# Performance work log

Measured on AMD Instinct MI355X. Metric: run time of the kernel, lower is better.

Reference implementation:

```python
import jax, jax.numpy as jnp
import numpy as np

NEG_SLOPE = 0.2
EPS = 1e-12


def setup_inputs() -> dict:
    key = jax.random.key(0)
    k1, k2, k3, k4, k5 = jax.random.split(key, 5)
    N, E, IN, OUT = 100000, 1600000, 256, 64
    x = jax.random.normal(k1, (N, IN), dtype=jnp.float32)
    edge_index = jax.random.randint(k2, (2, E), 0, N, dtype=jnp.int64)
    # GATConv (heads=1) parameters: lin weight, att_src, att_dst, bias
    W = jax.random.normal(k3, (IN, OUT), dtype=jnp.float32) * (1.0 / np.sqrt(IN))
    att_src = jax.random.normal(k4, (OUT,), dtype=jnp.float32) * (1.0 / np.sqrt(OUT))
    att_dst = jax.random.normal(k5, (OUT,), dtype=jnp.float32) * (1.0 / np.sqrt(OUT))
    bias = jnp.zeros((OUT,), dtype=jnp.float32)
    return {"x": x, "edge_index": edge_index, "W": W,
            "att_src": att_src, "att_dst": att_dst, "bias": bias}


def reference(x, edge_index, W, att_src, att_dst, bias):
    N = x.shape[0]
    # PyG GATConv default add_self_loops=True
    loops = jnp.arange(N, dtype=edge_index.dtype)
    src = jnp.concatenate([edge_index[0], loops])  # source j of edge (j -> i)
    dst = jnp.concatenate([edge_index[1], loops])  # target i (softmax segment)

    h = x @ W                                      # [N, out]
    a_src = h @ att_src                            # [N] per-node source score
    a_dst = h @ att_dst                            # [N] per-node target score

    e = jax.nn.leaky_relu(a_src[src] + a_dst[dst], NEG_SLOPE)  # [E+N]
    # segment softmax over incoming edges of each destination node
    e_max = jax.ops.segment_max(e, dst, num_segments=N)
    e = jnp.exp(e - e_max[dst])
    denom = jax.ops.segment_sum(e, dst, num_segments=N)
    alpha = e / denom[dst]                         # [E+N]

    # scatter-aggregate: out[i] = sum_j alpha_ij * h[j]
    out = jax.ops.segment_sum(alpha[:, None] * h[src], dst, num_segments=N)
    out = out + bias

    # dropout (p=0.3) in eval mode is identity; then F.normalize (row-wise L2)
    nrm = jnp.sqrt(jnp.sum(out * out, axis=-1, keepdims=True))
    return out / jnp.maximum(nrm, EPS)
```

## Files before the change

kernel.cpp:

```cpp
#include <hip/hip_runtime.h>
#include <hip/hip_bf16.h>
#include <math.h>

#define NEG_SLOPE 0.2f
#define EPS_NRM 1e-12f
#define K_IN 256
#define C_OUT 64

typedef __attribute__((ext_vector_type(8))) short bf16x8;
typedef __attribute__((ext_vector_type(4))) float f32x4;

__device__ __forceinline__ unsigned short bf16_rne(float v) {
    unsigned u = __float_as_uint(v);
    return (unsigned short)((u + 0x7fffu + ((u >> 16) & 1u)) >> 16);
}

__global__ __launch_bounds__(256) void wsplit(
    const float* __restrict__ W, unsigned short* __restrict__ Wt_hi,
    unsigned short* __restrict__ Wt_lo)
{
    int tid = blockIdx.x * blockDim.x + threadIdx.x;
    if (tid >= K_IN * C_OUT) return;
    int k = tid >> 6, c = tid & 63;
    float v = W[tid];
    unsigned short hb = bf16_rne(v);
    float vh = __uint_as_float((unsigned)hb << 16);
    unsigned short lb = bf16_rne(v - vh);
    Wt_hi[c * K_IN + k] = hb;
    Wt_lo[c * K_IN + k] = lb;
}

__global__ __launch_bounds__(256) void gemm_att(
    const float* __restrict__ x,
    const unsigned short* __restrict__ Wt_hi,
    const unsigned short* __restrict__ Wt_lo,
    const float* __restrict__ att_s, const float* __restrict__ att_d,
    __hip_bfloat16* __restrict__ h, float* __restrict__ a_src_arr,
    float* __restrict__ a_dst_arr, int N,
    const int* __restrict__ dstA, int* __restrict__ cnt, int E)
{
    int t   = threadIdx.x;
    int gw  = (blockIdx.x * blockDim.x + t) >> 6;
    int l   = t & 63;
    int lm  = l & 15;
    int grp = l >> 4;
    int row0 = gw * 16;

    int srow = row0 + lm; if (srow >= N) srow = N - 1;
    const float* xq = x + (size_t)srow * K_IN + grp * 8;

    const unsigned short* wbh = Wt_hi + (size_t)lm * K_IN + grp * 8;
    const unsigned short* wbl = Wt_lo + (size_t)lm * K_IN + grp * 8;

    f32x4 acc[4];
#pragma unroll
    for (int n = 0; n < 4; ++n) acc[n] = (f32x4){0.f, 0.f, 0.f, 0.f};

    float4 xa = *(const float4*)(xq);
    float4 xb = *(const float4*)(xq + 4);

    for (int kt = 0; kt < K_IN / 32; ++kt) {
        float4 xa2, xb2;
        if (kt < K_IN / 32 - 1) {
            xa2 = *(const float4*)(xq + (kt + 1) * 32);
            xb2 = *(const float4*)(xq + (kt + 1) * 32 + 4);
        }
        short sh[8], sl[8];
        const float* fa = (const float*)&xa;
        const float* fb = (const float*)&xb;
#pragma unroll
        for (int i = 0; i < 4; ++i) {
            float v0 = fa[i], v1 = fb[i];
            unsigned short h0 = bf16_rne(v0), h1 = bf16_rne(v1);
            sh[i] = (short)h0; sh[i + 4] = (short)h1;
            sl[i]     = (short)bf16_rne(v0 - __uint_as_float((unsigned)h0 << 16));
            sl[i + 4] = (short)bf16_rne(v1 - __uint_as_float((unsigned)h1 << 16));
        }
        bf16x8 xh = *(bf16x8*)&sh[0];
        bf16x8 xl = *(bf16x8*)&sl[0];

        int ko = kt * 32;
#pragma unroll
        for (int n = 0; n < 4; ++n) {
            bf16x8 wh = *(const bf16x8*)(wbh + (size_t)n * 16 * K_IN + ko);
            bf16x8 wl = *(const bf16x8*)(wbl + (size_t)n * 16 * K_IN + ko);
            acc[n] = __builtin_amdgcn_mfma_f32_16x16x32_bf16(wh, xh, acc[n], 0, 0, 0);
            acc[n] = __builtin_amdgcn_mfma_f32_16x16x32_bf16(wl, xh, acc[n], 0, 0, 0);
            acc[n] = __builtin_amdgcn_mfma_f32_16x16x32_bf16(wh, xl, acc[n], 0, 0, 0);
        }
        xa = xa2; xb = xb2;
    }

    int row = row0 + lm;
    float ps = 0.f, pd = 0.f;
#pragma unroll
    for (int n = 0; n < 4; ++n) {
        float4 as4 = *(const float4*)(att_s + n * 16 + grp * 4);
        float4 ad4 = *(const float4*)(att_d + n * 16 + grp * 4);
        f32x4 a = acc[n];
        ps += a.x * as4.x + a.y * as4.y + a.z * as4.z + a.w * as4.w;
        pd += a.x * ad4.x + a.y * ad4.y + a.z * ad4.z + a.w * ad4.w;
    }
    ps += __shfl_xor(ps, 16, 64); ps += __shfl_xor(ps, 32, 64);
    pd += __shfl_xor(pd, 16, 64); pd += __shfl_xor(pd, 32, 64);
    if (row < N) {
        if (grp == 0) { a_src_arr[row] = ps; a_dst_arr[row] = pd; }
#pragma unroll
        for (int n = 0; n < 4; ++n) {
            f32x4 a = acc[n];
            __hip_bfloat16 b0 = __float2bfloat16(a.x);
            __hip_bfloat16 b1 = __float2bfloat16(a.y);
            __hip_bfloat16 b2 = __float2bfloat16(a.z);
            __hip_bfloat16 b3 = __float2bfloat16(a.w);
            unsigned long long pk =
                (unsigned long long)*(unsigned short*)&b0 |
                ((unsigned long long)*(unsigned short*)&b1 << 16) |
                ((unsigned long long)*(unsigned short*)&b2 << 32) |
                ((unsigned long long)*(unsigned short*)&b3 << 48);
            *(unsigned long long*)(h + (size_t)row * C_OUT + n * 16 + grp * 4) = pk;
        }
    }

    int stride = gridDim.x * blockDim.x;
    for (int i = blockIdx.x * blockDim.x + t; i < E; i += stride)
        atomicAdd(&cnt[dstA[i]], 1);
}

__global__ __launch_bounds__(256) void scan_p1(
    const int* __restrict__ cnt, int* __restrict__ partials, int n)
{
    int b = blockIdx.x, t = threadIdx.x;
    int base = b * 1024;
    int s = 0;
#pragma unroll
    for (int j = 0; j < 4; ++j) {
        int i = base + t * 4 + j;
        if (i < n) s += cnt[i];
    }
    for (int d = 1; d < 64; d <<= 1) s += __shfl_xor(s, d, 64);
    __shared__ int wsum[4];
    int lane = t & 63, wid = t >> 6;
    if (lane == 0) wsum[wid] = s;
    __syncthreads();
    if (t == 0) partials[b] = wsum[0] + wsum[1] + wsum[2] + wsum[3];
}

__global__ __launch_bounds__(256) void scan_p2(int* partials, int nb)
{
    __shared__ int buf[256];
    int t = threadIdx.x;
    int v = (t < nb) ? partials[t] : 0;
    buf[t] = v;
    __syncthreads();
    for (int d = 1; d < 256; d <<= 1) {
        int w = (t >= d) ? buf[t - d] : 0;
        __syncthreads();
        buf[t] += w;
        __syncthreads();
    }
    if (t < nb) partials[t] = buf[t] - v;
}

__global__ __launch_bounds__(256) void scan_p3(
    const int* __restrict__ cnt, const int* __restrict__ partials,
    int* __restrict__ offsets, int n)
{
    int b = blockIdx.x, t = threadIdx.x;
    int base = b * 1024;
    int v[4];
    int s = 0;
#pragma unroll
    for (int j = 0; j < 4; ++j) {
        int i = base + t * 4 + j;
        v[j] = (i < n) ? cnt[i] : 0;
        s += v[j];
    }
    int lane = t & 63, wid = t >> 6;
    int incl = s;
    for (int d = 1; d < 64; d <<= 1) {
        int w = __shfl_up(incl, d, 64);
        if (lane >= d) incl += w;
    }
    __shared__ int wsum[4];
    __shared__ int wbase[4];
    if (lane == 63) wsum[wid] = incl;
    __syncthreads();
    if (t == 0) {
        int r = 0;
        for (int i = 0; i < 4; ++i) { wbase[i] = r; r += wsum[i]; }
    }
    __syncthreads();
    int run = partials[b] + wbase[wid] + (incl - s);
#pragma unroll
    for (int j = 0; j < 4; ++j) {
        int i = base + t * 4 + j;
        if (i < n) {
            offsets[i] = run;
            run += v[j];
            if (i == n - 1) offsets[n] = run;
        }
    }
}

__global__ __launch_bounds__(256) void scatter_edges(
    const int* __restrict__ srcA, const int* __restrict__ dstA,
    const int* __restrict__ offsets, int* __restrict__ cursor,
    const float* __restrict__ a_src, const float* __restrict__ a_dst,
    unsigned long long* __restrict__ csr, int E)
{
    int i = blockIdx.x * blockDim.x + threadIdx.x;
    if (i >= E) return;
    int s = srcA[i], d = dstA[i];
    float e = a_src[s] + a_dst[d];
    e = fmaxf(e, NEG_SLOPE * e);
    float w = __expf(e);
    int pos = offsets[d] + atomicAdd(&cursor[d], 1);
    unsigned long long packed =
        (unsigned long long)(unsigned)s |
        ((unsigned long long)__float_as_uint(w) << 32);
    __builtin_nontemporal_store(packed, &csr[pos]);
}

__global__ __launch_bounds__(256) void gat_pull(
    const int* __restrict__ offsets, const int2* __restrict__ csr,
    const unsigned short* __restrict__ h, const float* __restrict__ a_src,
    const float* __restrict__ a_dst, const float* __restrict__ bias,
    float* __restrict__ out, int N)
{
    int gw   = (blockIdx.x * blockDim.x + threadIdx.x) >> 6;
    int lane = threadIdx.x & 63;
    int grp  = lane >> 4;
    int gl   = lane & 15;
    int node = gw * 4 + grp;
    bool valid = node < N;
    int nv = valid ? node : 0;

    int beg = offsets[nv];
    int n   = valid ? (offsets[nv + 1] - beg) : 0;
    const int2* ce = csr + (n ? beg : 0);

    float asv = a_src[nv], adv = a_dst[nv];
    float es = asv + adv; es = fmaxf(es, NEG_SLOPE * es);
    float ws = __expf(es);
    unsigned long long hu = *(const unsigned long long*)
        (h + (size_t)nv * C_OUT + 4 * gl);
    unsigned hl = (unsigned)hu, hh = (unsigned)(hu >> 32);
    float acc0 = ws * __uint_as_float(hl << 16);
    float acc1 = ws * __uint_as_float(hl & 0xffff0000u);
    float acc2 = ws * __uint_as_float(hh << 16);
    float acc3 = ws * __uint_as_float(hh & 0xffff0000u);
    float den = ws;

    int2 c0 = ce[0];
    int2 c1 = ce[(n > 1) ? 1 : 0];
    unsigned long long u0 = *(const unsigned long long*)
        (h + (size_t)c0.x * C_OUT + 4 * gl);
    unsigned long long u1 = *(const unsigned long long*)
        (h + (size_t)c1.x * C_OUT + 4 * gl);

    for (int p = 0; p < n; p += 2) {
        int2 m0 = ce[(p + 2 < n) ? p + 2 : 0];
        int2 m1 = ce[(p + 3 < n) ? p + 3 : 0];
        unsigned long long v0 = *(const unsigned long long*)
            (h + (size_t)m0.x * C_OUT + 4 * gl);
        unsigned long long v1 = *(const unsigned long long*)
            (h + (size_t)m1.x * C_OUT + 4 * gl);

        float w0 = __int_as_float(c0.y);
        float w1 = (p + 1 < n) ? __int_as_float(c1.y) : 0.f;
        unsigned l0 = (unsigned)u0, h0 = (unsigned)(u0 >> 32);
        unsigned l1 = (unsigned)u1, h1 = (unsigned)(u1 >> 32);
        den  += w0 + w1;
        acc0 += w0 * __uint_as_float(l0 << 16)
              + w1 * __uint_as_float(l1 << 16);
        acc1 += w0 * __uint_as_float(l0 & 0xffff0000u)
              + w1 * __uint_as_float(l1 & 0xffff0000u);
        acc2 += w0 * __uint_as_float(h0 << 16)
              + w1 * __uint_as_float(h1 << 16);
        acc3 += w0 * __uint_as_float(h0 & 0xffff0000u)
              + w1 * __uint_as_float(h1 & 0xffff0000u);

        c0 = m0; c1 = m1; u0 = v0; u1 = v1;
    }

    float4 bl = *(const float4*)(bias + 4 * gl);
    float rd = 1.f / den;
    float o0 = acc0 * rd + bl.x;
    float o1 = acc1 * rd + bl.y;
    float o2 = acc2 * rd + bl.z;
    float o3 = acc3 * rd + bl.w;

    float sq = o0 * o0 + o1 * o1 + o2 * o2 + o3 * o3;
#pragma unroll
    for (int d = 1; d < 16; d <<= 1) sq += __shfl_xor(sq, d, 64);
    float rn = 1.f / fmaxf(sqrtf(sq), EPS_NRM);

    if (valid)
        *(float4*)(out + (size_t)node * C_OUT + 4 * gl) =
            make_float4(o0 * rn, o1 * rn, o2 * rn, o3 * rn);
}

extern "C" void kernel_launch(void* const* d_in, const int* in_sizes, int n_in,
                              void* d_out, int out_size, void* d_ws, size_t ws_size,
                              hipStream_t stream)
{
    const float* x     = (const float*)d_in[0];
    const int*   ei    = (const int*)d_in[1];
    const float* W     = (const float*)d_in[2];
    const float* att_s = (const float*)d_in[3];
    const float* att_d = (const float*)d_in[4];
    const float* bias  = (const float*)d_in[5];
    float*       out   = (float*)d_out;

    const int OUT = in_sizes[3];
    const int IN  = in_sizes[2] / OUT;
    const int N   = in_sizes[0] / IN;
    const int E   = in_sizes[1] / 2;

    char* w = (char*)d_ws;
    auto alloc = [&](size_t bytes) -> void* {
        void* p = (void*)w;
        w += (bytes + 255) & ~(size_t)255;
        return p;
    };
    __hip_bfloat16* h = (__hip_bfloat16*)alloc((size_t)N * C_OUT * 2);
    float* a_src  = (float*)alloc((size_t)N * 4);
    float* a_dst  = (float*)alloc((size_t)N * 4);
    int*   cnt    = (int*)alloc((size_t)N * 2 * 4);
    int*   offs   = (int*)alloc((size_t)(N + 1) * 4);
    int*   parts  = (int*)alloc(1024 * 4);
    unsigned short* Wt_hi = (unsigned short*)alloc((size_t)K_IN * C_OUT * 2);
    unsigned short* Wt_lo = (unsigned short*)alloc((size_t)K_IN * C_OUT * 2);
    unsigned long long* csr = (unsigned long long*)alloc((size_t)E * 8);
    int*   cursor = cnt + N;

    hipMemsetAsync(cnt, 0, (size_t)N * 2 * 4, stream);

    wsplit<<<(K_IN * C_OUT + 255) / 256, 256, 0, stream>>>(W, Wt_hi, Wt_lo);

    gemm_att<<<(N + 63) / 64, 256, 0, stream>>>(
        x, Wt_hi, Wt_lo, att_s, att_d, h, a_src, a_dst, N, ei + E, cnt, E);

    int NB = (N + 1023) / 1024;
    scan_p1<<<NB, 256, 0, stream>>>(cnt, parts, N);
    scan_p2<<<1, 256, 0, stream>>>(parts, NB);
    scan_p3<<<NB, 256, 0, stream>>>(cnt, parts, offs, N);

    scatter_edges<<<(E + 255) / 256, 256, 0, stream>>>(
        ei, ei + E, offs, cursor, a_src, a_dst, csr, E);

    gat_pull<<<(N + 15) / 16, 256, 0, stream>>>(offs, (const int2*)csr,
        (const unsigned short*)h, a_src, a_dst, bias, out, N);
}
```

Before: 387.4 us.

## Record per-edge rank from counting atomics to drop second atomic pass

The counting atomicAdd in gemm_att now keeps its return value as a per-edge rank, and scatter_edges uses offsets[d]+rank[i] instead of a second atomicAdd on a cursor array. The first four edge iterations are issued before the GEMM so their atomic latency overlaps the matrix work. This removes one full pass of contended atomics and the cursor memset, at the cost of writing and reading an extra E-sized int array and holding a few extra registers in the GEMM kernel.

Measured after the change: 374.0 us. 1.04x faster.

```diff
diff --git a/kernel.cpp b/kernel.cpp
--- a/kernel.cpp
+++ b/kernel.cpp
@@ -37,10 +37,24 @@
     const float* __restrict__ att_s, const float* __restrict__ att_d,
     __hip_bfloat16* __restrict__ h, float* __restrict__ a_src_arr,
     float* __restrict__ a_dst_arr, int N,
-    const int* __restrict__ dstA, int* __restrict__ cnt, int E)
-{
-    int t   = threadIdx.x;
-    int gw  = (blockIdx.x * blockDim.x + t) >> 6;
+    const int* __restrict__ dstA, int* __restrict__ cnt,
+    int* __restrict__ rank, int E)
+{
+    int t      = threadIdx.x;
+    int gtid   = blockIdx.x * blockDim.x + t;
+    int stride = gridDim.x * blockDim.x;
+
+    int r0 = 0, r1 = 0, r2 = 0, r3 = 0;
+    int i0 = gtid, i1 = gtid + stride, i2 = gtid + 2 * stride,
+        i3 = gtid + 3 * stride;
+    if (i0 < E) r0 = atomicAdd(&cnt[dstA[i0]], 1);
+    if (i1 < E) r1 = atomicAdd(&cnt[dstA[i1]], 1);
+    if (i2 < E) r2 = atomicAdd(&cnt[dstA[i2]], 1);
+    if (i3 < E) r3 = atomicAdd(&cnt[dstA[i3]], 1);
+    for (int i = gtid + 4 * stride; i < E; i += stride)
+        rank[i] = atomicAdd(&cnt[dstA[i]], 1);
+
+    int gw  = gtid >> 6;
     int l   = t & 63;
     int lm  = l & 15;
     int grp = l >> 4;
@@ -121,9 +135,10 @@
         }
     }
 
-    int stride = gridDim.x * blockDim.x;
-    for (int i = blockIdx.x * blockDim.x + t; i < E; i += stride)
-        atomicAdd(&cnt[dstA[i]], 1);
+    if (i0 < E) rank[i0] = r0;
+    if (i1 < E) rank[i1] = r1;
+    if (i2 < E) rank[i2] = r2;
+    if (i3 < E) rank[i3] = r3;
 }
 
 __global__ __launch_bounds__(256) void scan_p1(
@@ -204,7 +219,7 @@
 
 __global__ __launch_bounds__(256) void scatter_edges(
     const int* __restrict__ srcA, const int* __restrict__ dstA,
-    const int* __restrict__ offsets, int* __restrict__ cursor,
+    const int* __restrict__ offsets, const int* __restrict__ rank,
     const float* __restrict__ a_src, const float* __restrict__ a_dst,
     unsigned long long* __restrict__ csr, int E)
 {
@@ -214,7 +229,7 @@
     float e = a_src[s] + a_dst[d];
     e = fmaxf(e, NEG_SLOPE * e);
     float w = __expf(e);
-    int pos = offsets[d] + atomicAdd(&cursor[d], 1);
+    int pos = offsets[d] + rank[i];
     unsigned long long packed =
         (unsigned long long)(unsigned)s |
         ((unsigned long long)__float_as_uint(w) << 32);
@@ -326,20 +341,21 @@
     __hip_bfloat16* h = (__hip_bfloat16*)alloc((size_t)N * C_OUT * 2);
     float* a_src  = (float*)alloc((size_t)N * 4);
     float* a_dst  = (float*)alloc((size_t)N * 4);
-    int*   cnt    = (int*)alloc((size_t)N * 2 * 4);
+    int*   cnt    = (int*)alloc((size_t)N * 4);
     int*   offs   = (int*)alloc((size_t)(N + 1) * 4);
     int*   parts  = (int*)alloc(1024 * 4);
     unsigned short* Wt_hi = (unsigned short*)alloc((size_t)K_IN * C_OUT * 2);
     unsigned short* Wt_lo = (unsigned short*)alloc((size_t)K_IN * C_OUT * 2);
+    int*   rank   = (int*)alloc((size_t)E * 4);
     unsigned long long* csr = (unsigned long long*)alloc((size_t)E * 8);
-    int*   cursor = cnt + N;
-
-    hipMemsetAsync(cnt, 0, (size_t)N * 2 * 4, stream);
+
+    hipMemsetAsync(cnt, 0, (size_t)N * 4, stream);
 
     wsplit<<<(K_IN * C_OUT + 255) / 256, 256, 0, stream>>>(W, Wt_hi, Wt_lo);
 
     gemm_att<<<(N + 63) / 64, 256, 0, stream>>>(
-        x, Wt_hi, Wt_lo, att_s, att_d, h, a_src, a_dst, N, ei + E, cnt, E);
+        x, Wt_hi, Wt_lo, att_s, att_d, h, a_src, a_dst, N, ei + E, cnt,
+        rank, E);
 
     int NB = (N + 1023) / 1024;
     scan_p1<<<NB, 256, 0, stream>>>(cnt, parts, N);
@@ -347,7 +363,7 @@
     scan_p3<<<NB, 256, 0, stream>>>(cnt, parts, offs, N);
 
     scatter_edges<<<(E + 255) / 256, 256, 0, stream>>>(
-        ei, ei + E, offs, cursor, a_src, a_dst, csr, E);
+        ei, ei + E, offs, rank, a_src, a_dst, csr, E);
 
     gat_pull<<<(N + 15) / 16, 256, 0, stream>>>(offs, (const int2*)csr,
         (const unsigned short*)h, a_src, a_dst, bias, out, N);
```
